# Kernel optimization log

Hardware: AMD Instinct MI355X
Metric: run time of the kernel (lower is better)

Reference implementation:

```python
import jax, jax.numpy as jnp
import numpy as np

B, N, D = 8, 2048, 512

def setup_inputs() -> dict:
    key = jax.random.key(0)
    ks = jax.random.split(key, 8)
    s = 1.0 / np.sqrt(D)
    return {
        "inputs": jax.random.normal(ks[0], (B, N, D), dtype=jnp.float32),
        "mask": jnp.ones((B, N), dtype=jnp.int32),
        "Wk": jax.random.normal(ks[1], (D, D), dtype=jnp.float32) * s,
        "bk": jax.random.normal(ks[2], (D,), dtype=jnp.float32) * s,
        "Wq": jax.random.normal(ks[3], (D, D), dtype=jnp.float32) * s,
        "bq": jax.random.normal(ks[4], (D,), dtype=jnp.float32) * s,
        "Wv": jax.random.normal(ks[5], (D, D), dtype=jnp.float32) * s,
        "bv": jax.random.normal(ks[6], (D,), dtype=jnp.float32) * s,
    }

def reference(inputs, mask, Wk, bk, Wq, bq, Wv, bv):
    # torch Linear: y = x @ W.T + b
    keys = jnp.einsum('bnd,ed->bne', inputs, Wk) + bk
    queries = jnp.einsum('bnd,ed->bne', inputs, Wq) + bq
    values = jnp.einsum('bnd,ed->bne', inputs, Wv) + bv
    norm = jnp.sqrt(jnp.asarray(D, inputs.dtype))
    scores = jnp.einsum('bqd,bkd->bqk', queries, keys) / norm  # [B,N,N]
    scores = jnp.where(mask[:, None, :] == 0, jnp.asarray(-1e9, scores.dtype), scores)
    attn = jax.nn.softmax(scores, axis=-1)
    return jnp.einsum('bqk,bkd->bqd', attn, values)
```

## Files before the change

### kernel.cpp

```cpp
#include <hip/hip_runtime.h>
#include <hip/hip_bf16.h>


typedef __attribute__((ext_vector_type(8))) short short8;
typedef __attribute__((ext_vector_type(4))) float f32x4;

#define DEV __device__ __forceinline__
#define GLOBAL_AS __attribute__((address_space(1)))
#define LDS_AS __attribute__((address_space(3)))

static DEV ushort f2bs(float f) {
  union { float f; unsigned u; } x; x.f = f;
  unsigned r = (x.u + 0x7fffu + ((x.u >> 16) & 1u)) >> 16;
  return (ushort)r;
}

static DEV f32x4 mfma16(short8 a, short8 b, f32x4 c) {
  return __builtin_amdgcn_mfma_f32_16x16x32_bf16(a, b, c, 0, 0, 0);
}

static DEV void async16(const void* g, void* l) {
  __builtin_amdgcn_global_load_lds((const GLOBAL_AS void*)g, (LDS_AS void*)l, 16, 0, 0);
}

__global__ void convert_all(const float* __restrict__ wq, const float* __restrict__ wk,
                            const float* __restrict__ wv, const float* __restrict__ x,
                            ushort* __restrict__ wb, ushort* __restrict__ xb,
                            float* __restrict__ lde) {
  int i = blockIdx.x * 256 + threadIdx.x;
  if (i >= 2293760) {
    int off = (i - 2293760) * 4;
    float4 z; z.x = 0.f; z.y = 0.f; z.z = 0.f; z.w = 0.f;
    *(float4*)(lde + off) = z;
    return;
  }
  const float* src;
  ushort* dst;
  if (i < 196608) {
    int which = i >> 16;
    int off = (i & 65535) * 4;
    src = ((which == 0) ? wq : (which == 1) ? wk : wv) + off;
    dst = wb + (size_t)which * 262144 + off;
  } else {
    int off = (i - 196608) * 4;
    src = x + off;
    dst = xb + off;
  }
  float4 v = *(const float4*)src;
  ushort4 o;
  o.x = f2bs(v.x); o.y = f2bs(v.y); o.z = f2bs(v.z); o.w = f2bs(v.w);
  *(ushort4*)dst = o;
}

#define KLOOP_STAGE(Aptr, lda, Bptr, ldb)                                      \
  do {                                                                         \
    _Pragma("unroll")                                                          \
    for (int t = 0; t < 16; t++) {                                             \
      int rowbase = (t & 7) * 16 + wave * 4;                                   \
      int r = rowbase + (lane >> 4);                                           \
      int gc = (lane & 15) ^ (r & 15);                                         \
      if (t < 8)                                                               \
        async16((Aptr) + (size_t)(rowblk * 128 + r) * (lda) + kb + gc * 8,     \
                &As[rowbase * 128]);                                           \
      else                                                                     \
        async16((Bptr) + (size_t)(colblk * 128 + r) * (ldb) + kb + gc * 8,     \
                &Bs[rowbase * 128]);                                           \
    }                                                                          \
  } while (0)

#define KLOOP_MFMA()                                                           \
  do {                                                                         \
    _Pragma("unroll")                                                          \
    for (int ks = 0; ks < 4; ks++) {                                           \
      short8 af[4], bfr[4];                                                    \
      _Pragma("unroll")                                                        \
      for (int t = 0; t < 4; t++) {                                            \
        int ra = wm * 64 + t * 16 + c16;                                       \
        int rb = wn * 64 + t * 16 + c16;                                       \
        af[t]  = *(const short8*)&As[ra * 128 + (((ks * 4 + quad) ^ (ra & 15)) * 8)]; \
        bfr[t] = *(const short8*)&Bs[rb * 128 + (((ks * 4 + quad) ^ (rb & 15)) * 8)]; \
      }                                                                        \
      _Pragma("unroll")                                                        \
      for (int mt = 0; mt < 4; mt++)                                           \
        _Pragma("unroll")                                                      \
        for (int nt = 0; nt < 4; nt++)                                         \
          acc[mt][nt] = mfma16(af[mt], bfr[nt], acc[mt][nt]);                  \
    }                                                                          \
  } while (0)

__launch_bounds__(256, 2)
__global__ void qkv_gemm(const ushort* __restrict__ Xb, const ushort* __restrict__ Wb,
                         const float* __restrict__ bq, const float* __restrict__ bk,
                         const float* __restrict__ bv,
                         ushort* __restrict__ Qb, ushort* __restrict__ Kb,
                         ushort* __restrict__ Vtb) {
  const int rowblk = blockIdx.x;
  const int colblk = blockIdx.y;
  const int z = colblk >> 2;

  __shared__ ushort As[128 * 128];
  __shared__ ushort Bs[128 * 128];

  const int tid = threadIdx.x;
  const int wave = tid >> 6, lane = tid & 63, quad = lane >> 4, c16 = lane & 15;
  const int wm = wave & 1, wn = wave >> 1;

  f32x4 acc[4][4];
#pragma unroll
  for (int mt = 0; mt < 4; mt++)
#pragma unroll
    for (int nt = 0; nt < 4; nt++) acc[mt][nt] = (f32x4)0.0f;

  for (int kb = 0; kb < 512; kb += 128) {
    __syncthreads();
    KLOOP_STAGE(Xb, 512, Wb, 512);
    __syncthreads();
    KLOOP_MFMA();
  }

  const float* bias = (z == 0) ? bq : (z == 1) ? bk : bv;
  float bvals[4];
#pragma unroll
  for (int nt = 0; nt < 4; nt++) {
    int eg = colblk * 128 + wn * 64 + nt * 16 + c16;
    bvals[nt] = bias[eg & 511];
  }
  const float sc = (z == 0) ? 0.044194173824159216f : 1.0f;

  const int row0 = rowblk * 128 + wm * 64;
  const int col0 = colblk * 128 + wn * 64;
  if (z < 2) {
    ushort* O = (z == 0) ? Qb : Kb;
#pragma unroll
    for (int mt = 0; mt < 4; mt++)
#pragma unroll
      for (int nt = 0; nt < 4; nt++) {
        int el = (col0 + nt * 16 + c16) & 511;
#pragma unroll
        for (int r = 0; r < 4; r++) {
          int n = row0 + mt * 16 + quad * 4 + r;
          O[(size_t)n * 512 + el] = f2bs((acc[mt][nt][r] + bvals[nt]) * sc);
        }
      }
  } else {
#pragma unroll
    for (int mt = 0; mt < 4; mt++) {
      int grow = row0 + mt * 16 + quad * 4;
      int b = grow >> 11, n0 = grow & 2047;
#pragma unroll
      for (int nt = 0; nt < 4; nt++) {
        int el = (col0 + nt * 16 + c16) & 511;
        ushort4 o;
        o.x = f2bs(acc[mt][nt][0] + bvals[nt]);
        o.y = f2bs(acc[mt][nt][1] + bvals[nt]);
        o.z = f2bs(acc[mt][nt][2] + bvals[nt]);
        o.w = f2bs(acc[mt][nt][3] + bvals[nt]);
        *(ushort4*)(Vtb + ((size_t)b * 512 + el) * 2048 + n0) = o;
      }
    }
  }
}

__launch_bounds__(256, 2)
__global__ void gemm_s(const ushort* __restrict__ Kb, const ushort* __restrict__ Qb,
                       const int* __restrict__ mask, ushort* __restrict__ Pm,
                       float* __restrict__ l) {
  const int b = blockIdx.z;
  const int rowblk = blockIdx.x;
  const int colblk = blockIdx.y;
  const ushort* A  = Kb + (size_t)b * 2048 * 512;
  const ushort* Bq = Qb + (size_t)b * 2048 * 512;

  __shared__ ushort As[128 * 128];
  __shared__ ushort Bs[128 * 128];

  const int tid = threadIdx.x;
  const int wave = tid >> 6, lane = tid & 63, quad = lane >> 4, c16 = lane & 15;
  const int wm = wave & 1, wn = wave >> 1;

  f32x4 acc[4][4];
#pragma unroll
  for (int mt = 0; mt < 4; mt++)
#pragma unroll
    for (int nt = 0; nt < 4; nt++) acc[mt][nt] = (f32x4)0.0f;

  for (int kb = 0; kb < 512; kb += 128) {
    __syncthreads();
    KLOOP_STAGE(A, 512, Bq, 512);
    __syncthreads();
    KLOOP_MFMA();
  }

  const int row0 = rowblk * 128 + wm * 64;
  const int col0 = colblk * 128 + wn * 64;
  float lpart[4] = {0.0f, 0.0f, 0.0f, 0.0f};
#pragma unroll
  for (int mt = 0; mt < 4; mt++) {
    int key0 = row0 + mt * 16 + quad * 4;
    int4 mv = *(const int4*)&mask[b * 2048 + key0];
    float mf0 = mv.x ? 1.0f : 0.0f, mf1 = mv.y ? 1.0f : 0.0f;
    float mf2 = mv.z ? 1.0f : 0.0f, mf3 = mv.w ? 1.0f : 0.0f;
#pragma unroll
    for (int nt = 0; nt < 4; nt++) {
      int q = col0 + nt * 16 + c16;
      float p0 = __expf(acc[mt][nt][0]) * mf0;
      float p1 = __expf(acc[mt][nt][1]) * mf1;
      float p2 = __expf(acc[mt][nt][2]) * mf2;
      float p3 = __expf(acc[mt][nt][3]) * mf3;
      ushort4 o;
      o.x = f2bs(p0); o.y = f2bs(p1); o.z = f2bs(p2); o.w = f2bs(p3);
      *(ushort4*)(Pm + ((size_t)b * 2048 + q) * 2048 + key0) = o;
      lpart[nt] += p0 + p1 + p2 + p3;
    }
  }
#pragma unroll
  for (int nt = 0; nt < 4; nt++) {
    float v = lpart[nt];
    v += __shfl_xor(v, 16, 64);
    v += __shfl_xor(v, 32, 64);
    if (quad == 0) atomicAdd(&l[b * 2048 + col0 + nt * 16 + c16], v);
  }
}

__launch_bounds__(256, 2)
__global__ void gemm_o(const ushort* __restrict__ Pm, const ushort* __restrict__ Vtb,
                       const float* __restrict__ l, float* __restrict__ out) {
  const int b = blockIdx.z;
  const int rowblk = blockIdx.x;
  const int colblk = blockIdx.y;
  const ushort* A  = Pm  + (size_t)b * 2048 * 2048;
  const ushort* Bv = Vtb + (size_t)b * 512 * 2048;

  __shared__ ushort As[128 * 128];
  __shared__ ushort Bs[128 * 128];

  const int tid = threadIdx.x;
  const int wave = tid >> 6, lane = tid & 63, quad = lane >> 4, c16 = lane & 15;
  const int wm = wave & 1, wn = wave >> 1;

  f32x4 acc[4][4];
#pragma unroll
  for (int mt = 0; mt < 4; mt++)
#pragma unroll
    for (int nt = 0; nt < 4; nt++) acc[mt][nt] = (f32x4)0.0f;

  for (int kb = 0; kb < 2048; kb += 128) {
    __syncthreads();
    KLOOP_STAGE(A, 2048, Bv, 2048);
    __syncthreads();
    KLOOP_MFMA();
  }

  const int row0 = rowblk * 128 + wm * 64;
  const int col0 = colblk * 128 + wn * 64;
  float linv[4][4];
#pragma unroll
  for (int mt = 0; mt < 4; mt++)
#pragma unroll
    for (int r = 0; r < 4; r++)
      linv[mt][r] = 1.0f / l[b * 2048 + row0 + mt * 16 + quad * 4 + r];
#pragma unroll
  for (int mt = 0; mt < 4; mt++)
#pragma unroll
    for (int nt = 0; nt < 4; nt++) {
      int col = col0 + nt * 16 + c16;
#pragma unroll
      for (int r = 0; r < 4; r++) {
        int row = row0 + mt * 16 + quad * 4 + r;
        out[((size_t)b * 2048 + row) * 512 + col] = acc[mt][nt][r] * linv[mt][r];
      }
    }
}

extern "C" void kernel_launch(void* const* d_in, const int* in_sizes, int n_in,
                              void* d_out, int out_size, void* d_ws, size_t ws_size,
                              hipStream_t stream) {
  (void)in_sizes; (void)n_in; (void)out_size; (void)ws_size;
  const float* X    = (const float*)d_in[0];
  const int*   mask = (const int*)d_in[1];
  const float* Wk   = (const float*)d_in[2];
  const float* bk   = (const float*)d_in[3];
  const float* Wq   = (const float*)d_in[4];
  const float* bq   = (const float*)d_in[5];
  const float* Wv   = (const float*)d_in[6];
  const float* bv   = (const float*)d_in[7];
  float* out = (float*)d_out;

  ushort* ws  = (ushort*)d_ws;
  ushort* Pm  = ws;
  ushort* Xb  = ws;
  ushort* Wb  = ws + (size_t)33554432;
  ushort* Qb  = Wb + (size_t)786432;
  ushort* Kb  = Qb + (size_t)8388608;
  ushort* Vtb = Kb + (size_t)8388608;
  float*  lde = (float*)(Vtb + (size_t)8388608);

  convert_all<<<8976, 256, 0, stream>>>(Wq, Wk, Wv, X, Wb, Xb, lde);
  qkv_gemm<<<dim3(128, 12), 256, 0, stream>>>(Xb, Wb, bq, bk, bv, Qb, Kb, Vtb);
  gemm_s<<<dim3(16, 16, 8), 256, 0, stream>>>(Kb, Qb, mask, Pm, lde);
  gemm_o<<<dim3(16, 4, 8), 256, 0, stream>>>(Pm, Vtb, lde, out);
}
```

Measured before the change: 222.0 us.

## Fuse score, softmax and PV GEMMs into one flash-style attention kernel

```diff
diff --git a/kernel.cpp b/kernel.cpp
--- a/kernel.cpp
+++ b/kernel.cpp
@@ -25,15 +25,8 @@
 
 __global__ void convert_all(const float* __restrict__ wq, const float* __restrict__ wk,
                             const float* __restrict__ wv, const float* __restrict__ x,
-                            ushort* __restrict__ wb, ushort* __restrict__ xb,
-                            float* __restrict__ lde) {
+                            ushort* __restrict__ wb, ushort* __restrict__ xb) {
   int i = blockIdx.x * 256 + threadIdx.x;
-  if (i >= 2293760) {
-    int off = (i - 2293760) * 4;
-    float4 z; z.x = 0.f; z.y = 0.f; z.z = 0.f; z.w = 0.f;
-    *(float4*)(lde + off) = z;
-    return;
-  }
   const float* src;
   ushort* dst;
   if (i < 196608) {
@@ -161,115 +154,118 @@
   }
 }
 
-__launch_bounds__(256, 2)
-__global__ void gemm_s(const ushort* __restrict__ Kb, const ushort* __restrict__ Qb,
-                       const int* __restrict__ mask, ushort* __restrict__ Pm,
-                       float* __restrict__ l) {
-  const int b = blockIdx.z;
-  const int rowblk = blockIdx.x;
-  const int colblk = blockIdx.y;
-  const ushort* A  = Kb + (size_t)b * 2048 * 512;
-  const ushort* Bq = Qb + (size_t)b * 2048 * 512;
-
-  __shared__ ushort As[128 * 128];
-  __shared__ ushort Bs[128 * 128];
-
+__launch_bounds__(512, 2)
+__global__ void attn_fused(const ushort* __restrict__ Qb, const ushort* __restrict__ Kb,
+                           const ushort* __restrict__ Vtb, const int* __restrict__ mask,
+                           float* __restrict__ out) {
+  const int bid = blockIdx.x;
+  const int b = bid & 7;
+  const int qt = bid >> 3;
+  const int q0 = qt * 64;
   const int tid = threadIdx.x;
   const int wave = tid >> 6, lane = tid & 63, quad = lane >> 4, c16 = lane & 15;
-  const int wm = wave & 1, wn = wave >> 1;
-
-  f32x4 acc[4][4];
+  const int qs = (wave & 3) * 16;
+  const int kh = (wave >> 2) * 16;
+  const int d0 = wave * 64;
+
+  __shared__ ushort Ks[32 * 512];
+  __shared__ ushort Ps[64][40];
+  __shared__ float Lf[2][64];
+
+  short8 qf[16];
+  {
+    const ushort* qsrc = Qb + ((size_t)b * 2048 + q0 + qs + c16) * 512 + quad * 8;
+#pragma unroll
+    for (int ks = 0; ks < 16; ks++) qf[ks] = *(const short8*)(qsrc + ks * 32);
+  }
+
+  const ushort* Kbase = Kb + (size_t)b * 2048 * 512;
+#pragma unroll
+  for (int t = 0; t < 4; t++) {
+    int r = wave * 4 + t;
+    async16(Kbase + (size_t)r * 512 + ((lane ^ (r & 15)) * 8), &Ks[r * 512]);
+  }
+
+  f32x4 o_acc[4][4];
 #pragma unroll
   for (int mt = 0; mt < 4; mt++)
 #pragma unroll
-    for (int nt = 0; nt < 4; nt++) acc[mt][nt] = (f32x4)0.0f;
-
-  for (int kb = 0; kb < 512; kb += 128) {
-    __syncthreads();
-    KLOOP_STAGE(A, 512, Bq, 512);
-    __syncthreads();
-    KLOOP_MFMA();
-  }
-
-  const int row0 = rowblk * 128 + wm * 64;
-  const int col0 = colblk * 128 + wn * 64;
+    for (int nt = 0; nt < 4; nt++) o_acc[mt][nt] = (f32x4)0.0f;
   float lpart[4] = {0.0f, 0.0f, 0.0f, 0.0f};
+
+  __syncthreads();
+
+  for (int kt = 0; kt < 64; kt++) {
+    short8 vf[4];
+    {
+      const ushort* vsrc = Vtb + ((size_t)b * 512 + d0 + c16) * 2048 + kt * 32 + quad * 8;
+#pragma unroll
+      for (int nt = 0; nt < 4; nt++) vf[nt] = *(const short8*)(vsrc + (size_t)nt * 16 * 2048);
+    }
+    const float mf = mask[b * 2048 + kt * 32 + kh + c16] ? 1.0f : 0.0f;
+
+    f32x4 s = (f32x4)0.0f;
+#pragma unroll
+    for (int ks = 0; ks < 16; ks++) {
+      short8 kfrag = *(const short8*)&Ks[(kh + c16) * 512 + (((ks * 4 + quad) ^ c16) * 8)];
+      s = mfma16(qf[ks], kfrag, s);
+    }
+
+#pragma unroll
+    for (int r = 0; r < 4; r++) {
+      float p = __expf(s[r]) * mf;
+      lpart[r] += p;
+      Ps[qs + quad * 4 + r][kh + c16] = f2bs(p);
+    }
+
+    __syncthreads();
+
+    if (kt < 63) {
+#pragma unroll
+      for (int t = 0; t < 4; t++) {
+        int r = wave * 4 + t;
+        async16(Kbase + (size_t)((kt + 1) * 32 + r) * 512 + ((lane ^ (r & 15)) * 8),
+                &Ks[r * 512]);
+      }
+    }
+
+    short8 pa[4];
+#pragma unroll
+    for (int mt = 0; mt < 4; mt++)
+      pa[mt] = *(const short8*)&Ps[mt * 16 + c16][quad * 8];
+#pragma unroll
+    for (int nt = 0; nt < 4; nt++)
+#pragma unroll
+      for (int mt = 0; mt < 4; mt++)
+        o_acc[mt][nt] = mfma16(pa[mt], vf[nt], o_acc[mt][nt]);
+
+    __syncthreads();
+  }
+
+#pragma unroll
+  for (int r = 0; r < 4; r++) {
+    float v = lpart[r];
+    v += __shfl_xor(v, 1, 64);
+    v += __shfl_xor(v, 2, 64);
+    v += __shfl_xor(v, 4, 64);
+    v += __shfl_xor(v, 8, 64);
+    if (c16 == 0) Lf[wave >> 2][qs + quad * 4 + r] = v;
+  }
+  __syncthreads();
+
 #pragma unroll
   for (int mt = 0; mt < 4; mt++) {
-    int key0 = row0 + mt * 16 + quad * 4;
-    int4 mv = *(const int4*)&mask[b * 2048 + key0];
-    float mf0 = mv.x ? 1.0f : 0.0f, mf1 = mv.y ? 1.0f : 0.0f;
-    float mf2 = mv.z ? 1.0f : 0.0f, mf3 = mv.w ? 1.0f : 0.0f;
-#pragma unroll
-    for (int nt = 0; nt < 4; nt++) {
-      int q = col0 + nt * 16 + c16;
-      float p0 = __expf(acc[mt][nt][0]) * mf0;
-      float p1 = __expf(acc[mt][nt][1]) * mf1;
-      float p2 = __expf(acc[mt][nt][2]) * mf2;
-      float p3 = __expf(acc[mt][nt][3]) * mf3;
-      ushort4 o;
-      o.x = f2bs(p0); o.y = f2bs(p1); o.z = f2bs(p2); o.w = f2bs(p3);
-      *(ushort4*)(Pm + ((size_t)b * 2048 + q) * 2048 + key0) = o;
-      lpart[nt] += p0 + p1 + p2 + p3;
-    }
-  }
-#pragma unroll
-  for (int nt = 0; nt < 4; nt++) {
-    float v = lpart[nt];
-    v += __shfl_xor(v, 16, 64);
-    v += __shfl_xor(v, 32, 64);
-    if (quad == 0) atomicAdd(&l[b * 2048 + col0 + nt * 16 + c16], v);
-  }
-}
-
-__launch_bounds__(256, 2)
-__global__ void gemm_o(const ushort* __restrict__ Pm, const ushort* __restrict__ Vtb,
-                       const float* __restrict__ l, float* __restrict__ out) {
-  const int b = blockIdx.z;
-  const int rowblk = blockIdx.x;
-  const int colblk = blockIdx.y;
-  const ushort* A  = Pm  + (size_t)b * 2048 * 2048;
-  const ushort* Bv = Vtb + (size_t)b * 512 * 2048;
-
-  __shared__ ushort As[128 * 128];
-  __shared__ ushort Bs[128 * 128];
-
-  const int tid = threadIdx.x;
-  const int wave = tid >> 6, lane = tid & 63, quad = lane >> 4, c16 = lane & 15;
-  const int wm = wave & 1, wn = wave >> 1;
-
-  f32x4 acc[4][4];
-#pragma unroll
-  for (int mt = 0; mt < 4; mt++)
-#pragma unroll
-    for (int nt = 0; nt < 4; nt++) acc[mt][nt] = (f32x4)0.0f;
-
-  for (int kb = 0; kb < 2048; kb += 128) {
-    __syncthreads();
-    KLOOP_STAGE(A, 2048, Bv, 2048);
-    __syncthreads();
-    KLOOP_MFMA();
-  }
-
-  const int row0 = rowblk * 128 + wm * 64;
-  const int col0 = colblk * 128 + wn * 64;
-  float linv[4][4];
-#pragma unroll
-  for (int mt = 0; mt < 4; mt++)
-#pragma unroll
-    for (int r = 0; r < 4; r++)
-      linv[mt][r] = 1.0f / l[b * 2048 + row0 + mt * 16 + quad * 4 + r];
-#pragma unroll
-  for (int mt = 0; mt < 4; mt++)
-#pragma unroll
-    for (int nt = 0; nt < 4; nt++) {
-      int col = col0 + nt * 16 + c16;
-#pragma unroll
-      for (int r = 0; r < 4; r++) {
-        int row = row0 + mt * 16 + quad * 4 + r;
-        out[((size_t)b * 2048 + row) * 512 + col] = acc[mt][nt][r] * linv[mt][r];
-      }
-    }
+#pragma unroll
+    for (int r = 0; r < 4; r++) {
+      int row = mt * 16 + quad * 4 + r;
+      float li = 1.0f / (Lf[0][row] + Lf[1][row]);
+#pragma unroll
+      for (int nt = 0; nt < 4; nt++) {
+        int col = d0 + nt * 16 + c16;
+        out[((size_t)b * 2048 + q0 + row) * 512 + col] = o_acc[mt][nt][r] * li;
+      }
+    }
+  }
 }
 
 extern "C" void kernel_launch(void* const* d_in, const int* in_sizes, int n_in,
@@ -287,16 +283,13 @@
   float* out = (float*)d_out;
 
   ushort* ws  = (ushort*)d_ws;
-  ushort* Pm  = ws;
-  ushort* Xb  = ws;
-  ushort* Wb  = ws + (size_t)33554432;
-  ushort* Qb  = Wb + (size_t)786432;
+  ushort* Wb  = ws;
+  ushort* Xb  = Wb + (size_t)786432;
+  ushort* Qb  = Xb + (size_t)8388608;
   ushort* Kb  = Qb + (size_t)8388608;
   ushort* Vtb = Kb + (size_t)8388608;
-  float*  lde = (float*)(Vtb + (size_t)8388608);
-
-  convert_all<<<8976, 256, 0, stream>>>(Wq, Wk, Wv, X, Wb, Xb, lde);
+
+  convert_all<<<8960, 256, 0, stream>>>(Wq, Wk, Wv, X, Wb, Xb);
   qkv_gemm<<<dim3(128, 12), 256, 0, stream>>>(Xb, Wb, bq, bk, bv, Qb, Kb, Vtb);
-  gemm_s<<<dim3(16, 16, 8), 256, 0, stream>>>(Kb, Qb, mask, Pm, lde);
-  gemm_o<<<dim3(16, 4, 8), 256, 0, stream>>>(Pm, Vtb, lde, out);
-}
+  attn_fused<<<256, 512, 0, stream>>>(Qb, Kb, Vtb, mask, out);
+}
```

After: 262.2 us. 18.1% more time.

## Load B operand directly from global into registers, halve LDS K-tile

Applied to the files above, without the earlier changes.

```diff
diff --git a/kernel.cpp b/kernel.cpp
--- a/kernel.cpp
+++ b/kernel.cpp
@@ -52,43 +52,46 @@
   *(ushort4*)dst = o;
 }
 
-#define KLOOP_STAGE(Aptr, lda, Bptr, ldb)                                      \
+#define STAGE_A64(Aptr, lda)                                                   \
   do {                                                                         \
     _Pragma("unroll")                                                          \
-    for (int t = 0; t < 16; t++) {                                             \
-      int rowbase = (t & 7) * 16 + wave * 4;                                   \
-      int r = rowbase + (lane >> 4);                                           \
-      int gc = (lane & 15) ^ (r & 15);                                         \
-      if (t < 8)                                                               \
-        async16((Aptr) + (size_t)(rowblk * 128 + r) * (lda) + kb + gc * 8,     \
-                &As[rowbase * 128]);                                           \
-      else                                                                     \
-        async16((Bptr) + (size_t)(colblk * 128 + r) * (ldb) + kb + gc * 8,     \
-                &Bs[rowbase * 128]);                                           \
+    for (int t = 0; t < 4; t++) {                                              \
+      int rowbase = (wave * 4 + t) * 8;                                        \
+      int r = rowbase + (lane >> 3);                                           \
+      int gc = (lane & 7) ^ (r & 7);                                           \
+      async16((Aptr) + (size_t)(rowblk * 128 + r) * (lda) + kb + gc * 8,       \
+              &As[rowbase * 64]);                                              \
     }                                                                          \
   } while (0)
 
-#define KLOOP_MFMA()                                                           \
+#define LOAD_B64()                                                             \
   do {                                                                         \
     _Pragma("unroll")                                                          \
-    for (int ks = 0; ks < 4; ks++) {                                           \
-      short8 af[4], bfr[4];                                                    \
+    for (int kk = 0; kk < 2; kk++)                                             \
+      _Pragma("unroll")                                                        \
+      for (int nt = 0; nt < 4; nt++)                                           \
+        bfr[kk][nt] = *(const short8*)(brow[nt] + kb + kk * 32);               \
+  } while (0)
+
+#define MFMA64()                                                               \
+  do {                                                                         \
+    _Pragma("unroll")                                                          \
+    for (int kk = 0; kk < 2; kk++) {                                           \
+      short8 af[4];                                                            \
       _Pragma("unroll")                                                        \
       for (int t = 0; t < 4; t++) {                                            \
         int ra = wm * 64 + t * 16 + c16;                                       \
-        int rb = wn * 64 + t * 16 + c16;                                       \
-        af[t]  = *(const short8*)&As[ra * 128 + (((ks * 4 + quad) ^ (ra & 15)) * 8)]; \
-        bfr[t] = *(const short8*)&Bs[rb * 128 + (((ks * 4 + quad) ^ (rb & 15)) * 8)]; \
+        af[t] = *(const short8*)&As[ra * 64 + (((kk * 4 + quad) ^ (ra & 7)) * 8)]; \
       }                                                                        \
       _Pragma("unroll")                                                        \
       for (int mt = 0; mt < 4; mt++)                                           \
         _Pragma("unroll")                                                      \
         for (int nt = 0; nt < 4; nt++)                                         \
-          acc[mt][nt] = mfma16(af[mt], bfr[nt], acc[mt][nt]);                  \
+          acc[mt][nt] = mfma16(af[mt], bfr[kk][nt], acc[mt][nt]);              \
     }                                                                          \
   } while (0)
 
-__launch_bounds__(256, 2)
+__launch_bounds__(256, 3)
 __global__ void qkv_gemm(const ushort* __restrict__ Xb, const ushort* __restrict__ Wb,
                          const float* __restrict__ bq, const float* __restrict__ bk,
                          const float* __restrict__ bv,
@@ -98,24 +101,30 @@
   const int colblk = blockIdx.y;
   const int z = colblk >> 2;
 
-  __shared__ ushort As[128 * 128];
-  __shared__ ushort Bs[128 * 128];
+  __shared__ ushort As[128 * 64];
 
   const int tid = threadIdx.x;
   const int wave = tid >> 6, lane = tid & 63, quad = lane >> 4, c16 = lane & 15;
   const int wm = wave & 1, wn = wave >> 1;
 
+  const ushort* brow[4];
+#pragma unroll
+  for (int nt = 0; nt < 4; nt++)
+    brow[nt] = Wb + (size_t)(colblk * 128 + wn * 64 + nt * 16 + c16) * 512 + quad * 8;
+
   f32x4 acc[4][4];
 #pragma unroll
   for (int mt = 0; mt < 4; mt++)
 #pragma unroll
     for (int nt = 0; nt < 4; nt++) acc[mt][nt] = (f32x4)0.0f;
 
-  for (int kb = 0; kb < 512; kb += 128) {
-    __syncthreads();
-    KLOOP_STAGE(Xb, 512, Wb, 512);
-    __syncthreads();
-    KLOOP_MFMA();
+  for (int kb = 0; kb < 512; kb += 64) {
+    __syncthreads();
+    STAGE_A64(Xb, 512);
+    short8 bfr[2][4];
+    LOAD_B64();
+    __syncthreads();
+    MFMA64();
   }
 
   const float* bias = (z == 0) ? bq : (z == 1) ? bk : bv;
@@ -161,7 +170,7 @@
   }
 }
 
-__launch_bounds__(256, 2)
+__launch_bounds__(256, 3)
 __global__ void gemm_s(const ushort* __restrict__ Kb, const ushort* __restrict__ Qb,
                        const int* __restrict__ mask, ushort* __restrict__ Pm,
                        float* __restrict__ l) {
@@ -171,24 +180,30 @@
   const ushort* A  = Kb + (size_t)b * 2048 * 512;
   const ushort* Bq = Qb + (size_t)b * 2048 * 512;
 
-  __shared__ ushort As[128 * 128];
-  __shared__ ushort Bs[128 * 128];
+  __shared__ ushort As[128 * 64];
 
   const int tid = threadIdx.x;
   const int wave = tid >> 6, lane = tid & 63, quad = lane >> 4, c16 = lane & 15;
   const int wm = wave & 1, wn = wave >> 1;
 
+  const ushort* brow[4];
+#pragma unroll
+  for (int nt = 0; nt < 4; nt++)
+    brow[nt] = Bq + (size_t)(colblk * 128 + wn * 64 + nt * 16 + c16) * 512 + quad * 8;
+
   f32x4 acc[4][4];
 #pragma unroll
   for (int mt = 0; mt < 4; mt++)
 #pragma unroll
     for (int nt = 0; nt < 4; nt++) acc[mt][nt] = (f32x4)0.0f;
 
-  for (int kb = 0; kb < 512; kb += 128) {
-    __syncthreads();
-    KLOOP_STAGE(A, 512, Bq, 512);
-    __syncthreads();
-    KLOOP_MFMA();
+  for (int kb = 0; kb < 512; kb += 64) {
+    __syncthreads();
+    STAGE_A64(A, 512);
+    short8 bfr[2][4];
+    LOAD_B64();
+    __syncthreads();
+    MFMA64();
   }
 
   const int row0 = rowblk * 128 + wm * 64;
@@ -222,7 +237,7 @@
   }
 }
 
-__launch_bounds__(256, 2)
+__launch_bounds__(256, 3)
 __global__ void gemm_o(const ushort* __restrict__ Pm, const ushort* __restrict__ Vtb,
                        const float* __restrict__ l, float* __restrict__ out) {
   const int b = blockIdx.z;
@@ -231,24 +246,30 @@
   const ushort* A  = Pm  + (size_t)b * 2048 * 2048;
   const ushort* Bv = Vtb + (size_t)b * 512 * 2048;
 
-  __shared__ ushort As[128 * 128];
-  __shared__ ushort Bs[128 * 128];
+  __shared__ ushort As[128 * 64];
 
   const int tid = threadIdx.x;
   const int wave = tid >> 6, lane = tid & 63, quad = lane >> 4, c16 = lane & 15;
   const int wm = wave & 1, wn = wave >> 1;
 
+  const ushort* brow[4];
+#pragma unroll
+  for (int nt = 0; nt < 4; nt++)
+    brow[nt] = Bv + (size_t)(colblk * 128 + wn * 64 + nt * 16 + c16) * 2048 + quad * 8;
+
   f32x4 acc[4][4];
 #pragma unroll
   for (int mt = 0; mt < 4; mt++)
 #pragma unroll
     for (int nt = 0; nt < 4; nt++) acc[mt][nt] = (f32x4)0.0f;
 
-  for (int kb = 0; kb < 2048; kb += 128) {
-    __syncthreads();
-    KLOOP_STAGE(A, 2048, Bv, 2048);
-    __syncthreads();
-    KLOOP_MFMA();
+  for (int kb = 0; kb < 2048; kb += 64) {
+    __syncthreads();
+    STAGE_A64(A, 2048);
+    short8 bfr[2][4];
+    LOAD_B64();
+    __syncthreads();
+    MFMA64();
   }
 
   const int row0 = rowblk * 128 + wm * 64;
```

Result: slower. 310.6 us (+39.9%).
